# Performance work log

Hardware: AMD Instinct MI355X
Metric: run time of the kernel (lower is better)

Reference implementation:

```python
import jax, jax.numpy as jnp
import numpy as np

EPS = 1e-8

def setup_inputs() -> dict:
    key = jax.random.key(0)
    k1, k2, k3 = jax.random.split(key, 3)
    central_value = jax.random.normal(k1, (256, 512), dtype=jnp.float32)
    partial_deviations = jax.random.normal(k2, (256, 256, 512), dtype=jnp.float32)
    err = jax.random.uniform(k3, (256, 512), dtype=jnp.float32)
    return {"central_value": central_value, "partial_deviations": partial_deviations, "err": err}


def reference(central_value, partial_deviations, err):
    # calculate_range: zonotope interval bounds
    radius = jnp.sum(jnp.abs(partial_deviations), axis=1) + jnp.abs(err)  # (B, D)
    lower = central_value - radius
    upper = central_value + radius

    rl = jax.nn.relu(lower)
    ru = jax.nn.relu(upper)
    lam = (ru - rl) / (upper - lower + EPS)
    lam = jnp.where(lower >= 0, 1.0, lam)
    lam = jnp.where(upper < 0, 0.0, lam)
    lam = jnp.nan_to_num(lam, nan=0.0)
    lam = jnp.clip(lam, 0.0, 1.0)
    beta = (rl - lam * lower) * 0.5
    delta = jnp.abs(beta)

    # apply_linear_approx
    new_central = lam * central_value + beta                              # (B, D)
    scaled_pd = partial_deviations * lam[:, None, :]                      # (B, N, D)
    d = central_value.shape[-1]
    diag = delta[:, :, None] * jnp.eye(d, dtype=delta.dtype)              # diag_embed -> (B, D, D)
    new_pd = jnp.concatenate([scaled_pd, diag], axis=1)                   # (B, N+D, D)
    new_err = lam * err
    return (new_central, new_pd, new_err)
```

## Files before the change

kernel.cpp:

```cpp
#include <hip/hip_runtime.h>

#define BB 256
#define NN 256
#define DD 512

constexpr float EPSF = 1e-8f;
constexpr size_t PD_OFF = (size_t)BB * DD;
constexpr size_t NE_OFF = PD_OFF + (size_t)BB * (NN + DD) * DD;

__device__ __forceinline__ void relax1(float rad_noerr, float e, float c,
                                       float& lam, float& del,
                                       float& ncv, float& nev) {
    float rad = rad_noerr + fabsf(e);
    float lo = c - rad;
    float up = c + rad;
    float rl = fmaxf(lo, 0.f);
    float ru = fmaxf(up, 0.f);
    float l = (ru - rl) / (up - lo + EPSF);
    if (lo >= 0.f) l = 1.f;
    if (up <  0.f) l = 0.f;
    if (l != l)    l = 0.f;
    l = fminf(fmaxf(l, 0.f), 1.f);
    float beta = (rl - l * lo) * 0.5f;
    lam = l;
    del = fabsf(beta);
    ncv = l * c + beta;
    nev = l * e;
}

__global__ __launch_bounds__(256) void stats_kernel(
    const float* __restrict__ cv, const float* __restrict__ pd,
    const float* __restrict__ err, float* __restrict__ out,
    float* __restrict__ lam_ws, float* __restrict__ delta_ws)
{
    const int blk   = blockIdx.x;
    const int b     = blk >> 1;
    const int dbase = (blk & 1) * 256;
    const int tid   = threadIdx.x;
    const int d4    = tid & 63;
    const int nc    = tid >> 6;

    const float4* pdrow = (const float4*)(pd + (size_t)b * NN * DD + dbase);
    float4 acc = make_float4(0.f, 0.f, 0.f, 0.f);
    const int n0 = nc * 64;
#pragma unroll 8
    for (int k = 0; k < 64; ++k) {
        float4 v = pdrow[(size_t)(n0 + k) * (DD / 4) + d4];
        acc.x += fabsf(v.x); acc.y += fabsf(v.y);
        acc.z += fabsf(v.z); acc.w += fabsf(v.w);
    }

    __shared__ float4 part[4][64];
    part[nc][d4] = acc;
    __syncthreads();

    if (nc == 0) {
        float4 a0 = part[0][d4], a1 = part[1][d4], a2 = part[2][d4], a3 = part[3][d4];
        float rads[4] = {a0.x + a1.x + a2.x + a3.x,
                         a0.y + a1.y + a2.y + a3.y,
                         a0.z + a1.z + a2.z + a3.z,
                         a0.w + a1.w + a2.w + a3.w};
        const size_t base = (size_t)b * DD + dbase + d4 * 4;
        float4 ev = *(const float4*)(err + base);
        float4 cb = *(const float4*)(cv + base);
        float e[4] = {ev.x, ev.y, ev.z, ev.w};
        float c[4] = {cb.x, cb.y, cb.z, cb.w};
        float lamv[4], delv[4], ncv[4], nev[4];
#pragma unroll
        for (int j = 0; j < 4; ++j)
            relax1(rads[j], e[j], c[j], lamv[j], delv[j], ncv[j], nev[j]);

        *(float4*)(out + base)           = make_float4(ncv[0], ncv[1], ncv[2], ncv[3]);
        *(float4*)(out + NE_OFF + base)  = make_float4(nev[0], nev[1], nev[2], nev[3]);
        *(float4*)(lam_ws + base)        = make_float4(lamv[0], lamv[1], lamv[2], lamv[3]);
        *(float4*)(delta_ws + base)      = make_float4(delv[0], delv[1], delv[2], delv[3]);
    }
}

__global__ __launch_bounds__(256) void writepd_kernel(
    const float* __restrict__ pd,
    const float* __restrict__ lam_ws,
    const float* __restrict__ delta_ws,
    float4* __restrict__ outpd)
{
    const size_t total = (size_t)BB * (NN + DD) * (DD / 4);
    size_t idx = (size_t)blockIdx.x * blockDim.x + threadIdx.x;
    const size_t stride = (size_t)gridDim.x * blockDim.x;
    for (; idx < total; idx += stride) {
        const unsigned d4     = (unsigned)(idx & (DD / 4 - 1));
        const unsigned row_id = (unsigned)(idx >> 7);
        const unsigned b      = row_id / (NN + DD);
        const unsigned r      = row_id - b * (NN + DD);
        float4 o;
        if (r < NN) {
            float4 v = ((const float4*)pd)[((size_t)b * NN + r) * (DD / 4) + d4];
            float4 l = ((const float4*)lam_ws)[(size_t)b * (DD / 4) + d4];
            o = make_float4(v.x * l.x, v.y * l.y, v.z * l.z, v.w * l.w);
        } else {
            const unsigned i = r - NN;
            o = make_float4(0.f, 0.f, 0.f, 0.f);
            if ((i >> 2) == d4) {
                float dv = delta_ws[(size_t)b * DD + i];
                ((float*)&o)[i & 3] = dv;
            }
        }
        outpd[idx] = o;
    }
}

extern "C" void kernel_launch(void* const* d_in, const int* in_sizes, int n_in,
                              void* d_out, int out_size, void* d_ws, size_t ws_size,
                              hipStream_t stream) {
    const float* cv  = (const float*)d_in[0];
    const float* pd  = (const float*)d_in[1];
    const float* err = (const float*)d_in[2];
    float* out = (float*)d_out;

    float* lam_ws   = (float*)d_ws;
    float* delta_ws = lam_ws + (size_t)BB * DD;

    stats_kernel<<<dim3(BB * 2), dim3(256), 0, stream>>>(cv, pd, err, out, lam_ws, delta_ws);

    writepd_kernel<<<dim3(12288), dim3(256), 0, stream>>>(
        pd, lam_ws, delta_ws, (float4*)(out + PD_OFF));
}
```

Measured before the change: 532.9 us.

## Fuse radius reduction and output writes into one register-resident kernel

```diff
diff --git a/kernel.cpp b/kernel.cpp
--- a/kernel.cpp
+++ b/kernel.cpp
@@ -3,108 +3,101 @@
 #define BB 256
 #define NN 256
 #define DD 512
+#define RT (NN + DD)
 
 constexpr float EPSF = 1e-8f;
 constexpr size_t PD_OFF = (size_t)BB * DD;
-constexpr size_t NE_OFF = PD_OFF + (size_t)BB * (NN + DD) * DD;
+constexpr size_t NE_OFF = PD_OFF + (size_t)BB * RT * DD;
 
-__device__ __forceinline__ void relax1(float rad_noerr, float e, float c,
-                                       float& lam, float& del,
-                                       float& ncv, float& nev) {
-    float rad = rad_noerr + fabsf(e);
-    float lo = c - rad;
-    float up = c + rad;
-    float rl = fmaxf(lo, 0.f);
-    float ru = fmaxf(up, 0.f);
-    float l = (ru - rl) / (up - lo + EPSF);
-    if (lo >= 0.f) l = 1.f;
-    if (up <  0.f) l = 0.f;
-    if (l != l)    l = 0.f;
-    l = fminf(fmaxf(l, 0.f), 1.f);
-    float beta = (rl - l * lo) * 0.5f;
-    lam = l;
-    del = fabsf(beta);
-    ncv = l * c + beta;
-    nev = l * e;
+typedef float vfloat4 __attribute__((ext_vector_type(4)));
+
+__device__ __forceinline__ vfloat4 nt_load4(const vfloat4* p) {
+    return __builtin_nontemporal_load(p);
+}
+__device__ __forceinline__ void nt_store4(vfloat4* p, vfloat4 v) {
+    __builtin_nontemporal_store(v, p);
 }
 
-__global__ __launch_bounds__(256) void stats_kernel(
+__global__ __launch_bounds__(256) void fused_kernel(
     const float* __restrict__ cv, const float* __restrict__ pd,
-    const float* __restrict__ err, float* __restrict__ out,
-    float* __restrict__ lam_ws, float* __restrict__ delta_ws)
+    const float* __restrict__ err, float* __restrict__ out)
 {
-    const int blk   = blockIdx.x;
-    const int b     = blk >> 1;
-    const int dbase = (blk & 1) * 256;
+    const int bx    = blockIdx.x;
+    const int b     = bx >> 3;
+    const int dbase = (bx & 7) * 64;
     const int tid   = threadIdx.x;
-    const int d4    = tid & 63;
-    const int nc    = tid >> 6;
+    const int j     = tid & 15;
+    const int rb    = tid >> 4;
 
-    const float4* pdrow = (const float4*)(pd + (size_t)b * NN * DD + dbase);
-    float4 acc = make_float4(0.f, 0.f, 0.f, 0.f);
-    const int n0 = nc * 64;
-#pragma unroll 8
-    for (int k = 0; k < 64; ++k) {
-        float4 v = pdrow[(size_t)(n0 + k) * (DD / 4) + d4];
-        acc.x += fabsf(v.x); acc.y += fabsf(v.y);
-        acc.z += fabsf(v.z); acc.w += fabsf(v.w);
+    const vfloat4* pdb = (const vfloat4*)(pd + (size_t)b * NN * DD + dbase);
+    vfloat4 data[16];
+    float ax = 0.f, ay = 0.f, az = 0.f, aw = 0.f;
+#pragma unroll
+    for (int k = 0; k < 16; ++k) {
+        const int r = rb + (k << 4);
+        vfloat4 v = nt_load4(pdb + (size_t)r * (DD / 4) + j);
+        data[k] = v;
+        ax += fabsf(v.x); ay += fabsf(v.y); az += fabsf(v.z); aw += fabsf(v.w);
+    }
+    ax += __shfl_xor(ax, 16); ay += __shfl_xor(ay, 16);
+    az += __shfl_xor(az, 16); aw += __shfl_xor(aw, 16);
+    ax += __shfl_xor(ax, 32); ay += __shfl_xor(ay, 32);
+    az += __shfl_xor(az, 32); aw += __shfl_xor(aw, 32);
+
+    __shared__ float part[4][64];
+    __shared__ __align__(16) float lam_s[64];
+    __shared__ float del_s[64];
+    const int wave = tid >> 6;
+    const int lane = tid & 63;
+    if (lane < 16) {
+        part[wave][lane * 4 + 0] = ax;
+        part[wave][lane * 4 + 1] = ay;
+        part[wave][lane * 4 + 2] = az;
+        part[wave][lane * 4 + 3] = aw;
+    }
+    __syncthreads();
+
+    if (tid < 64) {
+        float rad = part[0][tid] + part[1][tid] + part[2][tid] + part[3][tid];
+        const size_t gi = (size_t)b * DD + dbase + tid;
+        const float c = cv[gi];
+        const float e = err[gi];
+        rad += fabsf(e);
+        const float lo = c - rad, up = c + rad;
+        const float rl = fmaxf(lo, 0.f), ru = fmaxf(up, 0.f);
+        float l = (ru - rl) / (up - lo + EPSF);
+        if (lo >= 0.f) l = 1.f;
+        if (up <  0.f) l = 0.f;
+        if (l != l)    l = 0.f;
+        l = fminf(fmaxf(l, 0.f), 1.f);
+        const float beta = (rl - l * lo) * 0.5f;
+        out[gi]          = l * c + beta;
+        out[NE_OFF + gi] = l * e;
+        lam_s[tid] = l;
+        del_s[tid] = fabsf(beta);
+    }
+    __syncthreads();
+
+    const vfloat4 lm = *(const vfloat4*)&lam_s[j * 4];
+    vfloat4* outb = (vfloat4*)(out + PD_OFF + (size_t)b * RT * DD + dbase);
+#pragma unroll
+    for (int k = 0; k < 16; ++k) {
+        const int r = rb + (k << 4);
+        vfloat4 v = data[k];
+        v.x *= lm.x; v.y *= lm.y; v.z *= lm.z; v.w *= lm.w;
+        nt_store4(outb + (size_t)r * (DD / 4) + j, v);
     }
 
-    __shared__ float4 part[4][64];
-    part[nc][d4] = acc;
-    __syncthreads();
-
-    if (nc == 0) {
-        float4 a0 = part[0][d4], a1 = part[1][d4], a2 = part[2][d4], a3 = part[3][d4];
-        float rads[4] = {a0.x + a1.x + a2.x + a3.x,
-                         a0.y + a1.y + a2.y + a3.y,
-                         a0.z + a1.z + a2.z + a3.z,
-                         a0.w + a1.w + a2.w + a3.w};
-        const size_t base = (size_t)b * DD + dbase + d4 * 4;
-        float4 ev = *(const float4*)(err + base);
-        float4 cb = *(const float4*)(cv + base);
-        float e[4] = {ev.x, ev.y, ev.z, ev.w};
-        float c[4] = {cb.x, cb.y, cb.z, cb.w};
-        float lamv[4], delv[4], ncv[4], nev[4];
+    vfloat4* diagb = (vfloat4*)(out + PD_OFF + (size_t)b * RT * DD
+                                + (size_t)NN * DD + dbase);
 #pragma unroll
-        for (int j = 0; j < 4; ++j)
-            relax1(rads[j], e[j], c[j], lamv[j], delv[j], ncv[j], nev[j]);
-
-        *(float4*)(out + base)           = make_float4(ncv[0], ncv[1], ncv[2], ncv[3]);
-        *(float4*)(out + NE_OFF + base)  = make_float4(nev[0], nev[1], nev[2], nev[3]);
-        *(float4*)(lam_ws + base)        = make_float4(lamv[0], lamv[1], lamv[2], lamv[3]);
-        *(float4*)(delta_ws + base)      = make_float4(delv[0], delv[1], delv[2], delv[3]);
-    }
-}
-
-__global__ __launch_bounds__(256) void writepd_kernel(
-    const float* __restrict__ pd,
-    const float* __restrict__ lam_ws,
-    const float* __restrict__ delta_ws,
-    float4* __restrict__ outpd)
-{
-    const size_t total = (size_t)BB * (NN + DD) * (DD / 4);
-    size_t idx = (size_t)blockIdx.x * blockDim.x + threadIdx.x;
-    const size_t stride = (size_t)gridDim.x * blockDim.x;
-    for (; idx < total; idx += stride) {
-        const unsigned d4     = (unsigned)(idx & (DD / 4 - 1));
-        const unsigned row_id = (unsigned)(idx >> 7);
-        const unsigned b      = row_id / (NN + DD);
-        const unsigned r      = row_id - b * (NN + DD);
-        float4 o;
-        if (r < NN) {
-            float4 v = ((const float4*)pd)[((size_t)b * NN + r) * (DD / 4) + d4];
-            float4 l = ((const float4*)lam_ws)[(size_t)b * (DD / 4) + d4];
-            o = make_float4(v.x * l.x, v.y * l.y, v.z * l.z, v.w * l.w);
-        } else {
-            const unsigned i = r - NN;
-            o = make_float4(0.f, 0.f, 0.f, 0.f);
-            if ((i >> 2) == d4) {
-                float dv = delta_ws[(size_t)b * DD + i];
-                ((float*)&o)[i & 3] = dv;
-            }
-        }
-        outpd[idx] = o;
+    for (int k = 0; k < 32; ++k) {
+        const int i  = rb + (k << 4);
+        vfloat4 v = (vfloat4)(0.f, 0.f, 0.f, 0.f);
+        const int ii = i - dbase;
+        if ((unsigned)ii < 64u && (ii >> 2) == j)
+            v[ii & 3] = del_s[ii];
+        nt_store4(diagb + (size_t)i * (DD / 4) + j, v);
     }
 }
 
@@ -116,11 +109,5 @@
     const float* err = (const float*)d_in[2];
     float* out = (float*)d_out;
 
-    float* lam_ws   = (float*)d_ws;
-    float* delta_ws = lam_ws + (size_t)BB * DD;
-
-    stats_kernel<<<dim3(BB * 2), dim3(256), 0, stream>>>(cv, pd, err, out, lam_ws, delta_ws);
-
-    writepd_kernel<<<dim3(12288), dim3(256), 0, stream>>>(
-        pd, lam_ws, delta_ws, (float4*)(out + PD_OFF));
+    fused_kernel<<<dim3(BB * 8), dim3(256), 0, stream>>>(cv, pd, err, out);
 }
```

Measured after the change: 492.9 us. -7.5%, faster.
